# Performance work log

Measured on AMD Instinct MI355X. Metric: run time of the kernel, lower is better.

Reference implementation:

```python
import jax, jax.numpy as jnp
import numpy as np


def setup_inputs() -> dict:
    B, N, D, M = 512, 128, 768, 32  # bags, num_class, embed_dim, max bag size
    rng = np.random.default_rng(0)
    sizes = rng.integers(8, 25, size=B)  # variable bag sizes in [8, 24], all <= M
    offsets = np.concatenate([[0], np.cumsum(sizes)]).astype(np.int32)
    nsum = int(offsets[-1])
    scope = np.stack([offsets[:-1], offsets[1:]], axis=1)  # (B, 2) [start, end)

    key = jax.random.key(0)
    k1, k2, k3 = jax.random.split(key, 3)
    rep = jax.random.normal(k1, (nsum, D), dtype=jnp.float32)
    fc_weight = jax.random.normal(k2, (N, D), dtype=jnp.float32) * 0.02
    fc_bias = jax.random.normal(k3, (N,), dtype=jnp.float32) * 0.02
    return {
        "rep": rep,
        "fc_weight": fc_weight,
        "fc_bias": fc_bias,
        "scope": jnp.asarray(scope),
        "max_bag": M,
    }


def reference(rep, fc_weight, fc_bias, scope, max_bag):
    """IntraBagAttention forward (train=False, bag_size=0 branch), ragged bags
    rewritten as padded/masked dense ops.

    rep:       (nsum, D) sentence-encoder outputs
    fc_weight: (N, D), fc_bias: (N,)
    scope:     (B, 2) int [start, end) per bag; max_bag: static int pad bound
    returns:   (B, N) per-relation bag scores
    """
    nsum = rep.shape[0]
    starts = scope[:, 0]
    sizes = scope[:, 1] - scope[:, 0]
    pos = jnp.arange(max_bag)
    idx = jnp.clip(starts[:, None] + pos[None, :], 0, nsum - 1)  # (B, M)
    valid = pos[None, :] < sizes[:, None]                        # (B, M)
    bag = rep[idx]                                               # (B, M, D)

    # att_score = rep @ fc.weight.data.T ; .data => no grad through this use
    w_att = jax.lax.stop_gradient(fc_weight)
    att = jnp.einsum('bmd,nd->bnm', bag, w_att)                  # (B, N, M)
    att = jnp.where(valid[:, None, :], att, -jnp.inf)
    sm = jax.nn.softmax(att, axis=-1)                            # per-bag softmax over sentences

    # weighted segment sum: one attended rep per relation per bag
    rfer = jnp.einsum('bnm,bmd->bnd', sm, bag)                   # (B, N, D)

    # fc(rep_for_each_rel) -> (B, N, N); softmax over classes; take diagonal
    full = jnp.einsum('bnd,kd->bnk', rfer, fc_weight) + fc_bias  # (B, N, N)
    probs = jax.nn.softmax(full, axis=-1)
    return jnp.diagonal(probs, axis1=1, axis2=2)                 # (B, N)
```

## Files before the change

kernel.cpp:

```cpp
#include <hip/hip_runtime.h>
#include <math.h>

#define B_BAGS 512
#define N_REL  128
#define D_DIM  768
#define M_BAG  32
#define KSTEPS 24
#define CSTEPS 12

typedef __attribute__((ext_vector_type(8))) short  bf16x8;
typedef __attribute__((ext_vector_type(4))) float  f32x4;

__device__ inline unsigned pack_hi(float f0, float f1) {
    return __builtin_amdgcn_perm(__float_as_uint(f1), __float_as_uint(f0), 0x07060302u);
}
__device__ inline float trunc_res(float f) {
    return f - __uint_as_float(__float_as_uint(f) & 0xFFFF0000u);
}

__global__ void build_bfrag(const float* __restrict__ W, unsigned* __restrict__ Bfrag) {
    int flat = blockIdx.x * 256 + threadIdx.x;
    int lane = flat & 63;
    int tile = (flat >> 6) & 7;
    int s    = flat >> 9;
    int n  = tile * 16 + (lane & 15);
    int k0 = s * 32 + (lane >> 4) * 8;
    const float* src = &W[n * D_DIM + k0];
    float f[8];
    #pragma unroll
    for (int j = 0; j < 8; ++j) f[j] = src[j];
    unsigned hi[4], lo[4];
    #pragma unroll
    for (int q = 0; q < 4; ++q) {
        hi[q] = pack_hi(f[2*q], f[2*q+1]);
        lo[q] = pack_hi(trunc_res(f[2*q]), trunc_res(f[2*q+1]));
    }
    unsigned base = (unsigned)(((s * 8 + tile) * 2) * 64 + lane) * 4;
    *(uint4*)&Bfrag[base]          = make_uint4(hi[0], hi[1], hi[2], hi[3]);
    *(uint4*)&Bfrag[base + 64 * 4] = make_uint4(lo[0], lo[1], lo[2], lo[3]);
}

__global__ __launch_bounds__(256, 2) void bag_attn(
    const float*  __restrict__ rep,
    const float*  __restrict__ bias,
    const int*    __restrict__ scope,
    const unsigned short* __restrict__ Bfrag,
    float*        __restrict__ out,
    int nsum)
{
    __shared__ unsigned AhS[CSTEPS * 2 * 65 * 4];
    __shared__ unsigned AlS[CSTEPS * 2 * 65 * 4];
    __shared__ float Gs[M_BAG][N_REL + 4];
    __shared__ float redM[256], redL[256], redD[256];

    const int t = threadIdx.x;
    const int b = blockIdx.x;
    const int start = scope[2 * b];
    const int size  = scope[2 * b + 1] - start;

    const int wv   = t >> 6;
    const int lane = t & 63;

    f32x4 acc[2][2][3];
    #pragma unroll
    for (int h = 0; h < 2; ++h)
        #pragma unroll
        for (int tt = 0; tt < 2; ++tt)
            #pragma unroll
            for (int q = 0; q < 3; ++q)
                acc[h][tt][q] = f32x4{0.f, 0.f, 0.f, 0.f};

    const int m_st = t >> 3;
    const int r_st = t & 7;
    int row = start + m_st;
    row = (row > nsum - 1) ? (nsum - 1) : row;
    const float* rp0 = &rep[(size_t)row * D_DIM];

    for (int c = 0; c < 2; ++c) {
        const float* rp = rp0 + c * 384;
        #pragma unroll
        for (int i = 0; i < 6; ++i) {
            const int kk8 = r_st + 8 * i;
            const float4 v0 = *(const float4*)&rp[kk8 * 8];
            const float4 v1 = *(const float4*)&rp[kk8 * 8 + 4];
            const int s  = kk8 >> 2;
            const int kg = kk8 & 3;
            const int dst = ((s * 2 + (m_st >> 4)) * 65 + kg * 16 + (m_st & 15)) * 4;
            *(uint4*)&AhS[dst] = make_uint4(
                pack_hi(v0.x, v0.y), pack_hi(v0.z, v0.w),
                pack_hi(v1.x, v1.y), pack_hi(v1.z, v1.w));
            *(uint4*)&AlS[dst] = make_uint4(
                pack_hi(trunc_res(v0.x), trunc_res(v0.y)),
                pack_hi(trunc_res(v0.z), trunc_res(v0.w)),
                pack_hi(trunc_res(v1.x), trunc_res(v1.y)),
                pack_hi(trunc_res(v1.z), trunc_res(v1.w)));
        }
        __syncthreads();

        #pragma unroll 4
        for (int s = 0; s < CSTEPS; ++s) {
            const int gs = c * CSTEPS + s;
            const bf16x8 ah0 = *(const bf16x8*)&AhS[((s * 2 + 0) * 65 + lane) * 4];
            const bf16x8 ah1 = *(const bf16x8*)&AhS[((s * 2 + 1) * 65 + lane) * 4];
            const bf16x8 al0 = *(const bf16x8*)&AlS[((s * 2 + 0) * 65 + lane) * 4];
            const bf16x8 al1 = *(const bf16x8*)&AlS[((s * 2 + 1) * 65 + lane) * 4];
            #pragma unroll
            for (int tt = 0; tt < 2; ++tt) {
                const int tid8 = gs * 8 + (wv * 2 + tt);
                const bf16x8 bh = *(const bf16x8*)&Bfrag[(unsigned)((tid8 * 2 + 0) * 64 + lane) * 8];
                const bf16x8 bl = *(const bf16x8*)&Bfrag[(unsigned)((tid8 * 2 + 1) * 64 + lane) * 8];
                acc[0][tt][0] = __builtin_amdgcn_mfma_f32_16x16x32_bf16(ah0, bh, acc[0][tt][0], 0, 0, 0);
                acc[1][tt][0] = __builtin_amdgcn_mfma_f32_16x16x32_bf16(ah1, bh, acc[1][tt][0], 0, 0, 0);
                acc[0][tt][1] = __builtin_amdgcn_mfma_f32_16x16x32_bf16(ah0, bl, acc[0][tt][1], 0, 0, 0);
                acc[1][tt][1] = __builtin_amdgcn_mfma_f32_16x16x32_bf16(ah1, bl, acc[1][tt][1], 0, 0, 0);
                acc[0][tt][2] = __builtin_amdgcn_mfma_f32_16x16x32_bf16(al0, bh, acc[0][tt][2], 0, 0, 0);
                acc[1][tt][2] = __builtin_amdgcn_mfma_f32_16x16x32_bf16(al1, bh, acc[1][tt][2], 0, 0, 0);
            }
        }
        __syncthreads();
    }

    #pragma unroll
    for (int h = 0; h < 2; ++h)
        #pragma unroll
        for (int tt = 0; tt < 2; ++tt) {
            const f32x4 cw = acc[h][tt][0] + acc[h][tt][1] + acc[h][tt][2];
            const int n    = wv * 32 + tt * 16 + (lane & 15);
            const int mrow = h * 16 + (lane >> 4) * 4;
            #pragma unroll
            for (int rg = 0; rg < 4; ++rg) Gs[mrow + rg][n] = cw[rg];
        }
    __syncthreads();

    const int n = t & 127;
    const int h = t >> 7;

    float sm[M_BAG];
    float gmax = -INFINITY;
    #pragma unroll
    for (int m = 0; m < M_BAG; ++m) {
        float g = Gs[m][n];
        sm[m] = g;
        if (m < size) gmax = fmaxf(gmax, g);
    }
    float ssum = 0.f;
    #pragma unroll
    for (int m = 0; m < M_BAG; ++m) {
        float e = __expf(sm[m] - gmax);
        e = (m < size) ? e : 0.f;
        sm[m] = e;
        ssum += e;
    }
    const float inv = 1.f / ssum;
    #pragma unroll
    for (int m = 0; m < M_BAG; ++m) sm[m] *= inv;

    float mx = -INFINITY, l = 0.f, sd = 0.f;
    const int kbase = h * 64;
    #pragma unroll 4
    for (int kk = 0; kk < 64; kk += 4) {
        const int k = kbase + kk;
        float4 b4 = *(const float4*)&bias[k];
        float s0 = b4.x, s1 = b4.y, s2 = b4.z, s3 = b4.w;
        #pragma unroll
        for (int m = 0; m < M_BAG; ++m) {
            const float4 g = *(const float4*)&Gs[m][k];
            const float w = sm[m];
            s0 += w * g.x; s1 += w * g.y; s2 += w * g.z; s3 += w * g.w;
        }
        float s[4] = {s0, s1, s2, s3};
        #pragma unroll
        for (int j = 0; j < 4; ++j) {
            const float sj = s[j];
            const float mnew = fmaxf(mx, sj);
            l = l * __expf(mx - mnew) + __expf(sj - mnew);
            mx = mnew;
            sd = (k + j == n) ? sj : sd;
        }
    }

    redM[t] = mx; redL[t] = l; redD[t] = sd;
    __syncthreads();
    if (t < 128) {
        const float m0 = redM[t],       l0 = redL[t],       d0 = redD[t];
        const float m1 = redM[t + 128], l1 = redL[t + 128], d1 = redD[t + 128];
        const float M  = fmaxf(m0, m1);
        const float L  = l0 * __expf(m0 - M) + l1 * __expf(m1 - M);
        const float sdiag = (t < 64) ? d0 : d1;
        out[b * N_REL + t] = __expf(sdiag - M) / L;
    }
}

extern "C" void kernel_launch(void* const* d_in, const int* in_sizes, int n_in,
                              void* d_out, int out_size, void* d_ws, size_t ws_size,
                              hipStream_t stream) {
    const float* rep   = (const float*)d_in[0];
    const float* W     = (const float*)d_in[1];
    const float* bias  = (const float*)d_in[2];
    const int*   scope = (const int*)d_in[3];

    const int nsum = in_sizes[0] / D_DIM;
    unsigned* Bfrag = (unsigned*)d_ws;

    build_bfrag<<<48, 256, 0, stream>>>(W, Bfrag);
    bag_attn<<<B_BAGS, 256, 0, stream>>>(rep, bias, scope,
                                         (const unsigned short*)Bfrag,
                                         (float*)d_out, nsum);
}
```

Before: 113.7 us.

## Split into dense rep@W GEMM over real rows plus per-bag softmax kernel

Replaces the per-bag fused kernel, which padded each bag to 32 rows, with a standalone split-K MFMA GEMM over only the real nsum rows. Its results are accumulated into a global H buffer with atomics, and a second per-bag kernel then does both softmaxes on up to 24 rows. This removes wasted MFMA work on padded rows and uses three bf16 split products instead of the previous per-bag scheme. The cost is a memset, float atomics, an extra H round-trip through global memory, and the assumption that bag size never exceeds 24.

```diff
diff --git a/kernel.cpp b/kernel.cpp
--- a/kernel.cpp
+++ b/kernel.cpp
@@ -4,9 +4,9 @@
 #define B_BAGS 512
 #define N_REL  128
 #define D_DIM  768
-#define M_BAG  32
-#define KSTEPS 24
-#define CSTEPS 12
+#define M_PAD  24
+#define NCHUNK 8
+#define SPC    3
 
 typedef __attribute__((ext_vector_type(8))) short  bf16x8;
 typedef __attribute__((ext_vector_type(4))) float  f32x4;
@@ -40,17 +40,72 @@
     *(uint4*)&Bfrag[base + 64 * 4] = make_uint4(lo[0], lo[1], lo[2], lo[3]);
 }
 
-__global__ __launch_bounds__(256, 2) void bag_attn(
-    const float*  __restrict__ rep,
-    const float*  __restrict__ bias,
-    const int*    __restrict__ scope,
+__global__ __launch_bounds__(64) void h_gemm(
+    const float*          __restrict__ rep,
     const unsigned short* __restrict__ Bfrag,
-    float*        __restrict__ out,
+    float*                __restrict__ H,
     int nsum)
 {
-    __shared__ unsigned AhS[CSTEPS * 2 * 65 * 4];
-    __shared__ unsigned AlS[CSTEPS * 2 * 65 * 4];
-    __shared__ float Gs[M_BAG][N_REL + 4];
+    const int lane  = threadIdx.x;
+    const int strip = blockIdx.x;
+    const int chunk = blockIdx.y;
+
+    int row = strip * 16 + (lane & 15);
+    row = (row > nsum - 1) ? (nsum - 1) : row;
+    const float* rp = &rep[(size_t)row * D_DIM + (lane >> 4) * 8];
+
+    f32x4 acc[8][2];
+    #pragma unroll
+    for (int t = 0; t < 8; ++t) {
+        acc[t][0] = f32x4{0.f, 0.f, 0.f, 0.f};
+        acc[t][1] = f32x4{0.f, 0.f, 0.f, 0.f};
+    }
+
+    #pragma unroll
+    for (int s = 0; s < SPC; ++s) {
+        const int gs = chunk * SPC + s;
+        const float4 v0 = *(const float4*)&rp[gs * 32];
+        const float4 v1 = *(const float4*)&rp[gs * 32 + 4];
+        union { unsigned u[4]; bf16x8 v; } ah, al;
+        ah.u[0] = pack_hi(v0.x, v0.y);
+        ah.u[1] = pack_hi(v0.z, v0.w);
+        ah.u[2] = pack_hi(v1.x, v1.y);
+        ah.u[3] = pack_hi(v1.z, v1.w);
+        al.u[0] = pack_hi(trunc_res(v0.x), trunc_res(v0.y));
+        al.u[1] = pack_hi(trunc_res(v0.z), trunc_res(v0.w));
+        al.u[2] = pack_hi(trunc_res(v1.x), trunc_res(v1.y));
+        al.u[3] = pack_hi(trunc_res(v1.z), trunc_res(v1.w));
+
+        #pragma unroll
+        for (int tile = 0; tile < 8; ++tile) {
+            const int tid8 = gs * 8 + tile;
+            const bf16x8 bh = *(const bf16x8*)&Bfrag[((size_t)(tid8 * 2 + 0) * 64 + lane) * 8];
+            const bf16x8 bl = *(const bf16x8*)&Bfrag[((size_t)(tid8 * 2 + 1) * 64 + lane) * 8];
+            acc[tile][0] = __builtin_amdgcn_mfma_f32_16x16x32_bf16(ah.v, bh, acc[tile][0], 0, 0, 0);
+            acc[tile][1] = __builtin_amdgcn_mfma_f32_16x16x32_bf16(ah.v, bl, acc[tile][1], 0, 0, 0);
+            acc[tile][1] = __builtin_amdgcn_mfma_f32_16x16x32_bf16(al.v, bh, acc[tile][1], 0, 0, 0);
+        }
+    }
+
+    const int rowb = strip * 16 + (lane >> 4) * 4;
+    const int colb = lane & 15;
+    #pragma unroll
+    for (int tile = 0; tile < 8; ++tile) {
+        #pragma unroll
+        for (int r = 0; r < 4; ++r) {
+            atomicAdd(&H[(size_t)(rowb + r) * N_REL + tile * 16 + colb],
+                      acc[tile][0][r] + acc[tile][1][r]);
+        }
+    }
+}
+
+__global__ __launch_bounds__(256, 2) void bag_out(
+    const float* __restrict__ H,
+    const float* __restrict__ bias,
+    const int*   __restrict__ scope,
+    float*       __restrict__ out)
+{
+    __shared__ float Gs[M_PAD][N_REL + 4];
     __shared__ float redM[256], redL[256], redD[256];
 
     const int t = threadIdx.x;
@@ -58,94 +113,31 @@
     const int start = scope[2 * b];
     const int size  = scope[2 * b + 1] - start;
 
-    const int wv   = t >> 6;
-    const int lane = t & 63;
-
-    f32x4 acc[2][2][3];
-    #pragma unroll
-    for (int h = 0; h < 2; ++h)
-        #pragma unroll
-        for (int tt = 0; tt < 2; ++tt)
-            #pragma unroll
-            for (int q = 0; q < 3; ++q)
-                acc[h][tt][q] = f32x4{0.f, 0.f, 0.f, 0.f};
-
-    const int m_st = t >> 3;
-    const int r_st = t & 7;
-    int row = start + m_st;
-    row = (row > nsum - 1) ? (nsum - 1) : row;
-    const float* rp0 = &rep[(size_t)row * D_DIM];
-
-    for (int c = 0; c < 2; ++c) {
-        const float* rp = rp0 + c * 384;
-        #pragma unroll
-        for (int i = 0; i < 6; ++i) {
-            const int kk8 = r_st + 8 * i;
-            const float4 v0 = *(const float4*)&rp[kk8 * 8];
-            const float4 v1 = *(const float4*)&rp[kk8 * 8 + 4];
-            const int s  = kk8 >> 2;
-            const int kg = kk8 & 3;
-            const int dst = ((s * 2 + (m_st >> 4)) * 65 + kg * 16 + (m_st & 15)) * 4;
-            *(uint4*)&AhS[dst] = make_uint4(
-                pack_hi(v0.x, v0.y), pack_hi(v0.z, v0.w),
-                pack_hi(v1.x, v1.y), pack_hi(v1.z, v1.w));
-            *(uint4*)&AlS[dst] = make_uint4(
-                pack_hi(trunc_res(v0.x), trunc_res(v0.y)),
-                pack_hi(trunc_res(v0.z), trunc_res(v0.w)),
-                pack_hi(trunc_res(v1.x), trunc_res(v1.y)),
-                pack_hi(trunc_res(v1.z), trunc_res(v1.w)));
-        }
-        __syncthreads();
-
-        #pragma unroll 4
-        for (int s = 0; s < CSTEPS; ++s) {
-            const int gs = c * CSTEPS + s;
-            const bf16x8 ah0 = *(const bf16x8*)&AhS[((s * 2 + 0) * 65 + lane) * 4];
-            const bf16x8 ah1 = *(const bf16x8*)&AhS[((s * 2 + 1) * 65 + lane) * 4];
-            const bf16x8 al0 = *(const bf16x8*)&AlS[((s * 2 + 0) * 65 + lane) * 4];
-            const bf16x8 al1 = *(const bf16x8*)&AlS[((s * 2 + 1) * 65 + lane) * 4];
-            #pragma unroll
-            for (int tt = 0; tt < 2; ++tt) {
-                const int tid8 = gs * 8 + (wv * 2 + tt);
-                const bf16x8 bh = *(const bf16x8*)&Bfrag[(unsigned)((tid8 * 2 + 0) * 64 + lane) * 8];
-                const bf16x8 bl = *(const bf16x8*)&Bfrag[(unsigned)((tid8 * 2 + 1) * 64 + lane) * 8];
-                acc[0][tt][0] = __builtin_amdgcn_mfma_f32_16x16x32_bf16(ah0, bh, acc[0][tt][0], 0, 0, 0);
-                acc[1][tt][0] = __builtin_amdgcn_mfma_f32_16x16x32_bf16(ah1, bh, acc[1][tt][0], 0, 0, 0);
-                acc[0][tt][1] = __builtin_amdgcn_mfma_f32_16x16x32_bf16(ah0, bl, acc[0][tt][1], 0, 0, 0);
-                acc[1][tt][1] = __builtin_amdgcn_mfma_f32_16x16x32_bf16(ah1, bl, acc[1][tt][1], 0, 0, 0);
-                acc[0][tt][2] = __builtin_amdgcn_mfma_f32_16x16x32_bf16(al0, bh, acc[0][tt][2], 0, 0, 0);
-                acc[1][tt][2] = __builtin_amdgcn_mfma_f32_16x16x32_bf16(al1, bh, acc[1][tt][2], 0, 0, 0);
-            }
-        }
-        __syncthreads();
-    }
-
-    #pragma unroll
-    for (int h = 0; h < 2; ++h)
-        #pragma unroll
-        for (int tt = 0; tt < 2; ++tt) {
-            const f32x4 cw = acc[h][tt][0] + acc[h][tt][1] + acc[h][tt][2];
-            const int n    = wv * 32 + tt * 16 + (lane & 15);
-            const int mrow = h * 16 + (lane >> 4) * 4;
-            #pragma unroll
-            for (int rg = 0; rg < 4; ++rg) Gs[mrow + rg][n] = cw[rg];
-        }
+    #pragma unroll
+    for (int i = 0; i < 3; ++i) {
+        int flat = i * 256 + t;
+        int m  = flat >> 5;
+        int c4 = flat & 31;
+        float4 v = make_float4(0.f, 0.f, 0.f, 0.f);
+        if (m < size) v = *(const float4*)&H[(size_t)(start + m) * N_REL + c4 * 4];
+        *(float4*)&Gs[m][c4 * 4] = v;
+    }
     __syncthreads();
 
     const int n = t & 127;
     const int h = t >> 7;
 
-    float sm[M_BAG];
+    float sm[M_PAD];
     float gmax = -INFINITY;
     #pragma unroll
-    for (int m = 0; m < M_BAG; ++m) {
+    for (int m = 0; m < M_PAD; ++m) {
         float g = Gs[m][n];
         sm[m] = g;
         if (m < size) gmax = fmaxf(gmax, g);
     }
     float ssum = 0.f;
     #pragma unroll
-    for (int m = 0; m < M_BAG; ++m) {
+    for (int m = 0; m < M_PAD; ++m) {
         float e = __expf(sm[m] - gmax);
         e = (m < size) ? e : 0.f;
         sm[m] = e;
@@ -153,7 +145,7 @@
     }
     const float inv = 1.f / ssum;
     #pragma unroll
-    for (int m = 0; m < M_BAG; ++m) sm[m] *= inv;
+    for (int m = 0; m < M_PAD; ++m) sm[m] *= inv;
 
     float mx = -INFINITY, l = 0.f, sd = 0.f;
     const int kbase = h * 64;
@@ -163,7 +155,7 @@
         float4 b4 = *(const float4*)&bias[k];
         float s0 = b4.x, s1 = b4.y, s2 = b4.z, s3 = b4.w;
         #pragma unroll
-        for (int m = 0; m < M_BAG; ++m) {
+        for (int m = 0; m < M_PAD; ++m) {
             const float4 g = *(const float4*)&Gs[m][k];
             const float w = sm[m];
             s0 += w * g.x; s1 += w * g.y; s2 += w * g.z; s3 += w * g.w;
@@ -199,11 +191,15 @@
     const float* bias  = (const float*)d_in[2];
     const int*   scope = (const int*)d_in[3];
 
-    const int nsum = in_sizes[0] / D_DIM;
+    const int nsum   = in_sizes[0] / D_DIM;
+    const int strips = (nsum + 15) >> 4;
+
     unsigned* Bfrag = (unsigned*)d_ws;
+    float*    H     = (float*)((char*)d_ws + 393216);
 
     build_bfrag<<<48, 256, 0, stream>>>(W, Bfrag);
-    bag_attn<<<B_BAGS, 256, 0, stream>>>(rep, bias, scope,
-                                         (const unsigned short*)Bfrag,
-                                         (float*)d_out, nsum);
-}
+    hipMemsetAsync(H, 0, (size_t)strips * 16 * N_REL * sizeof(float), stream);
+    h_gemm<<<dim3(strips, NCHUNK), 64, 0, stream>>>(
+        rep, (const unsigned short*)Bfrag, H, nsum);
+    bag_out<<<B_BAGS, 256, 0, stream>>>(H, bias, scope, (float*)d_out);
+}
```

Result: slower. 123.8 us (+8.9%).
